# Performance work log

Hardware: AMD Instinct MI355X
Metric: run time of the kernel (lower is better)

## Reference

```python
import jax, jax.numpy as jnp
import numpy as np

N_NODES = 100000
N_EDGES = 1600000
F_IN = 128
HIDDEN = 128
N_CLASSES = 2
N_GRAPHS = 512


def setup_inputs() -> dict:
    key = jax.random.key(0)
    ks = jax.random.split(key, 10)
    node_features = jax.random.normal(ks[0], (N_NODES, F_IN), dtype=jnp.float32)
    edge_index = jax.random.randint(ks[1], (2, N_EDGES), 0, N_NODES, dtype=jnp.int64)
    batch = jnp.sort(jax.random.randint(ks[2], (N_NODES,), 0, N_GRAPHS, dtype=jnp.int64))
    s1 = 1.0 / np.sqrt(F_IN)
    s2 = 1.0 / np.sqrt(HIDDEN)
    W1 = jax.random.uniform(ks[3], (F_IN, HIDDEN), jnp.float32, -s1, s1)
    b1 = jnp.zeros((HIDDEN,), jnp.float32)
    W2 = jax.random.uniform(ks[4], (HIDDEN, HIDDEN), jnp.float32, -s2, s2)
    b2 = jnp.zeros((HIDDEN,), jnp.float32)
    Wlin = jax.random.uniform(ks[5], (HIDDEN, N_CLASSES), jnp.float32, -s2, s2)
    blin = jax.random.uniform(ks[6], (N_CLASSES,), jnp.float32, -s2, s2)
    return {"node_features": node_features, "edge_index": edge_index, "batch": batch,
            "W1": W1, "b1": b1, "W2": W2, "b2": b2, "Wlin": Wlin, "blin": blin}


def _gcn_conv(x, src, dst, norm, W, b, n_nodes):
    # transform-then-propagate (PyG GCNConv default)
    h = x @ W                                   # [N, H]
    msg = h[src] * norm[:, None]                # gather + edge scale
    out = jax.ops.segment_sum(msg, dst, num_segments=n_nodes)  # scatter-add
    return out + b


def reference(node_features, edge_index, batch, W1, b1, W2, b2, Wlin, blin):
    n = node_features.shape[0]
    loop = jnp.arange(n, dtype=edge_index.dtype)
    src = jnp.concatenate([edge_index[0], loop])  # add self-loops
    dst = jnp.concatenate([edge_index[1], loop])
    # symmetric degree normalization: deg counts incoming edges incl. self-loop
    deg = jax.ops.segment_sum(jnp.ones_like(src, dtype=node_features.dtype), dst, num_segments=n)
    dis = jnp.where(deg > 0, jax.lax.rsqrt(jnp.maximum(deg, 1.0)), 0.0)
    norm = dis[src] * dis[dst]

    x = jax.nn.relu(_gcn_conv(node_features, src, dst, norm, W1, b1, n))
    x = jax.nn.relu(_gcn_conv(x, src, dst, norm, W2, b2, n))

    # global mean pool over graphs
    ones = jnp.ones((n,), dtype=x.dtype)
    counts = jax.ops.segment_sum(ones, batch, num_segments=N_GRAPHS)
    sums = jax.ops.segment_sum(x, batch, num_segments=N_GRAPHS)
    pooled = sums / jnp.maximum(counts, 1.0)[:, None]

    # dropout is identity in eval mode
    return pooled @ Wlin + blin
```

## Files before the change

### kernel.cpp

```cpp
#include <hip/hip_runtime.h>
#include <hip/hip_bf16.h>
#include <hip/hip_fp16.h>

constexpr int NN = 100000;
constexpr int NE = 1600000;
constexpr int NG = 512;
constexpr int F  = 128;

constexpr int NB   = 392;
constexpr int RCAP = 4608;
constexpr int CAP  = 32;
constexpr int NCH  = 8;
constexpr int BINB = 512;
constexpr int GEMB = (NN + 127) / 128;

typedef _Float16 f16;
typedef f16 f16x2 __attribute__((ext_vector_type(2)));
typedef f16 f16x4 __attribute__((ext_vector_type(4)));
typedef f16 f16x8 __attribute__((ext_vector_type(8)));
typedef float f32x4 __attribute__((ext_vector_type(4)));
typedef unsigned int u32;
typedef u32 u32x4a __attribute__((ext_vector_type(4), aligned(4)));

__global__ __launch_bounds__(256) void k1_bin_prepw(const int* __restrict__ ei,
                                                    int* __restrict__ gcur,
                                                    u32* __restrict__ binned,
                                                    const float* __restrict__ W1,
                                                    const float* __restrict__ W2,
                                                    f16* __restrict__ WT1,
                                                    f16* __restrict__ WT2) {
    __shared__ u32 stage[NB][CAP];
    __shared__ int scnt[NB];
    if (blockIdx.x >= BINB) {
        int idx = (blockIdx.x - BINB) * 256 + threadIdx.x;
        int n = idx >> 7, k = idx & 127;
        WT1[idx] = (f16)W1[k * 128 + n];
        WT2[idx] = (f16)W2[k * 128 + n];
        return;
    }
    for (int b = threadIdx.x; b < NB; b += 256) scnt[b] = 0;
    __syncthreads();
    const int per = NE / BINB;
    const int e0 = blockIdx.x * per;
    for (int r = 0; r < per; r += 256) {
        int k = r + threadIdx.x;
        if (k < per) {
            int e = e0 + k;
            int s = __builtin_nontemporal_load(&ei[e]);
            int d = __builtin_nontemporal_load(&ei[NE + e]);
            int b = d >> 8;
            u32 v = ((u32)(d & 255) << 24) | (u32)s;
            int p = atomicAdd(&scnt[b], 1);
            if (p < CAP) stage[b][p] = v;
        }
        __syncthreads();
        for (int b2 = threadIdx.x; b2 < NB; b2 += 256) {
            int n = scnt[b2];
            if (n >= 16) {
                int f = n & ~15;
                int base = b2 * RCAP + atomicAdd(&gcur[b2], f);
                const u32x4a* st4 = (const u32x4a*)&stage[b2][0];
                u32x4a* out4 = (u32x4a*)&binned[base];
                for (int j = 0; j < (f >> 2); j++) out4[j] = st4[j];
                for (int j = 0; j < n - f; j++) stage[b2][j] = stage[b2][f + j];
                scnt[b2] = n - f;
            }
        }
        __syncthreads();
    }
    for (int b2 = threadIdx.x; b2 < NB; b2 += 256) {
        int n = scnt[b2];
        if (n > 0) {
            int base = b2 * RCAP + atomicAdd(&gcur[b2], n);
            for (int j = 0; j < n; j++) binned[base + j] = stage[b2][j];
        }
    }
}

template<bool IN_HALF, bool SCALE>
__device__ __forceinline__ void gemm_body(int bid, int tid,
                                          const void* __restrict__ Xv,
                                          const f16* __restrict__ WT,
                                          const float* __restrict__ dis,
                                          f16* __restrict__ H, int M) {
    const int wid = tid >> 6;
    const int lane = tid & 63;
    const int row0 = bid * 128;
    const int wrow = wid * 32;
    const int lr = lane & 15;
    const int lk = (lane >> 4) * 8;
    f32x4 acc[2][8] = {};
    #pragma unroll
    for (int ks = 0; ks < 4; ks++) {
        f16x8 a[2], b[8];
        #pragma unroll
        for (int mf = 0; mf < 2; mf++) {
            int row = row0 + wrow + mf * 16 + lr;
            row = row < M ? row : M - 1;
            if (IN_HALF) {
                a[mf] = *(const f16x8*)((const f16*)Xv + (size_t)row * 128 + ks * 32 + lk);
            } else {
                const float* Xf = (const float*)Xv + (size_t)row * 128 + ks * 32 + lk;
                float4 v0 = *(const float4*)Xf;
                float4 v1 = *(const float4*)(Xf + 4);
                a[mf] = f16x8{(f16)v0.x, (f16)v0.y, (f16)v0.z, (f16)v0.w,
                              (f16)v1.x, (f16)v1.y, (f16)v1.z, (f16)v1.w};
            }
        }
        #pragma unroll
        for (int nf = 0; nf < 8; nf++)
            b[nf] = *(const f16x8*)(WT + (size_t)(nf * 16 + lr) * 128 + ks * 32 + lk);
        #pragma unroll
        for (int mf = 0; mf < 2; mf++)
            #pragma unroll
            for (int nf = 0; nf < 8; nf++)
                acc[mf][nf] = __builtin_amdgcn_mfma_f32_16x16x32_f16(a[mf], b[nf], acc[mf][nf], 0, 0, 0);
    }
    const int crow = (lane >> 4) * 4;
    #pragma unroll
    for (int mf = 0; mf < 2; mf++) {
        #pragma unroll
        for (int reg = 0; reg < 4; reg++) {
            int row = row0 + wrow + mf * 16 + crow + reg;
            if (row < M) {
                float sc = SCALE ? dis[row] : 1.0f;
                #pragma unroll
                for (int nf = 0; nf < 8; nf++)
                    H[(size_t)row * 128 + nf * 16 + lr] = (f16)(acc[mf][nf][reg] * sc);
            }
        }
    }
}

__global__ __launch_bounds__(256) void k2_csr_gemm1(const u32* __restrict__ binned,
                                                    const int* __restrict__ gcur,
                                                    int* __restrict__ offs,
                                                    float* __restrict__ dis,
                                                    int* __restrict__ csr_src,
                                                    const float* __restrict__ X,
                                                    const f16* __restrict__ WT1,
                                                    f16* __restrict__ H) {
    __shared__ u32 ed[RCAP];
    __shared__ u32 lcsr[RCAP];
    __shared__ int hist[256];
    __shared__ int loff[256];
    __shared__ int lcur[256];
    if (blockIdx.x >= NB) {
        gemm_body<false, false>(blockIdx.x - NB, threadIdx.x, X, WT1, nullptr, H, NN);
        return;
    }
    const int b = blockIdx.x;
    const int t = threadIdx.x;
    {
        int c0 = (t < b) ? gcur[t] : 0;
        int c1 = (t + 256 < b) ? gcur[t + 256] : 0;
        loff[t] = c0 + c1;
        __syncthreads();
        for (int d = 128; d > 0; d >>= 1) {
            if (t < d) loff[t] += loff[t + d];
            __syncthreads();
        }
    }
    const int gbase = loff[0];
    __syncthreads();
    int cnt = gcur[b];
    if (cnt > RCAP) cnt = RCAP;
    hist[t] = 0;
    if (b == 0 && t == 0) offs[NN] = NE;
    __syncthreads();
    for (int j = t; j < cnt; j += 256) {
        u32 v = __builtin_nontemporal_load(&binned[(size_t)b * RCAP + j]);
        ed[j] = v;
        atomicAdd(&hist[v >> 24], 1);
    }
    __syncthreads();
    int h = hist[t];
    loff[t] = h;
    __syncthreads();
    for (int d = 1; d < 256; d <<= 1) {
        int x = (t >= d) ? loff[t - d] : 0;
        __syncthreads();
        loff[t] += x;
        __syncthreads();
    }
    int excl = loff[t] - h;
    lcur[t] = excl;
    int node = (b << 8) + t;
    if (node < NN) {
        offs[node] = gbase + excl;
        dis[node] = rsqrtf((float)(h + 1));
    }
    __syncthreads();
    for (int j = t; j < cnt; j += 256) {
        u32 v = ed[j];
        int p = atomicAdd(&lcur[v >> 24], 1);
        lcsr[p] = v & 0x1FFFFu;
    }
    __syncthreads();
    for (int j = t; j < cnt; j += 256) csr_src[gbase + j] = (int)lcsr[j];
}

__device__ __forceinline__ void gather_rows_scaled(const f16* __restrict__ h, int i,
                                                   const int* __restrict__ offs,
                                                   const int* __restrict__ csr_src,
                                                   const float* __restrict__ dis,
                                                   int q, int r, float acc[8]) {
    if (q == 0) {
        f16x8 v = *(const f16x8*)(h + (size_t)i * F + r * 8);
        float di = dis[i];
        #pragma unroll
        for (int j = 0; j < 8; j++) acc[j] = (float)v[j] * di;
    }
    const int s = offs[i], e = offs[i + 1];
    int t = s + q;
    for (; t + 4 < e; t += 8) {
        int sr0 = csr_src[t];
        int sr1 = csr_src[t + 4];
        float d0 = dis[sr0], d1 = dis[sr1];
        f16x8 v0 = *(const f16x8*)(h + (size_t)sr0 * F + r * 8);
        f16x8 v1 = *(const f16x8*)(h + (size_t)sr1 * F + r * 8);
        #pragma unroll
        for (int j = 0; j < 8; j++)
            acc[j] += (float)v0[j] * d0 + (float)v1[j] * d1;
    }
    if (t < e) {
        int sr = csr_src[t];
        float d0 = dis[sr];
        f16x8 v = *(const f16x8*)(h + (size_t)sr * F + r * 8);
        #pragma unroll
        for (int j = 0; j < 8; j++) acc[j] += (float)v[j] * d0;
    }
    #pragma unroll
    for (int j = 0; j < 8; j++) {
        acc[j] += __shfl_xor(acc[j], 16);
        acc[j] += __shfl_xor(acc[j], 32);
    }
}

__device__ __forceinline__ void gather_rows(const f16* __restrict__ h, int i,
                                            const int* __restrict__ offs,
                                            const int* __restrict__ csr_src,
                                            int q, int r, float acc[8]) {
    if (q == 0) {
        f16x8 v = *(const f16x8*)(h + (size_t)i * F + r * 8);
        #pragma unroll
        for (int j = 0; j < 8; j++) acc[j] = (float)v[j];
    }
    const int s = offs[i], e = offs[i + 1];
    int t = s + q;
    for (; t + 4 < e; t += 8) {
        int sr0 = csr_src[t];
        int sr1 = csr_src[t + 4];
        f16x8 v0 = *(const f16x8*)(h + (size_t)sr0 * F + r * 8);
        f16x8 v1 = *(const f16x8*)(h + (size_t)sr1 * F + r * 8);
        #pragma unroll
        for (int j = 0; j < 8; j++) acc[j] += (float)v0[j] + (float)v1[j];
    }
    if (t < e) {
        int sr = csr_src[t];
        f16x8 v = *(const f16x8*)(h + (size_t)sr * F + r * 8);
        #pragma unroll
        for (int j = 0; j < 8; j++) acc[j] += (float)v[j];
    }
    #pragma unroll
    for (int j = 0; j < 8; j++) {
        acc[j] += __shfl_xor(acc[j], 16);
        acc[j] += __shfl_xor(acc[j], 32);
    }
}

__global__ __launch_bounds__(256) void aggregate_l1(const f16* __restrict__ h,
                                                    const int* __restrict__ offs,
                                                    const int* __restrict__ csr_src,
                                                    const float* __restrict__ dis,
                                                    const float* __restrict__ bias,
                                                    f16* __restrict__ out, int n) {
    int i = blockIdx.x * 4 + (threadIdx.x >> 6);
    if (i >= n) return;
    const int lane = threadIdx.x & 63;
    const int q = lane >> 4;
    const int r = lane & 15;
    float acc[8] = {};
    gather_rows_scaled(h, i, offs, csr_src, dis, q, r, acc);
    if (q == 0) {
        float di = dis[i];
        const float4* b4 = (const float4*)bias;
        float4 bb0 = b4[r * 2], bb1 = b4[r * 2 + 1];
        float bb[8] = {bb0.x, bb0.y, bb0.z, bb0.w, bb1.x, bb1.y, bb1.z, bb1.w};
        f16x8 o;
        #pragma unroll
        for (int j = 0; j < 8; j++) {
            float v = fmaf(acc[j], di, bb[j]);
            o[j] = (f16)(v > 0.f ? v : 0.f);
        }
        *(f16x8*)(out + (size_t)i * F + r * 8) = o;
    }
}

__global__ __launch_bounds__(256) void aggregate_l2(const f16* __restrict__ h,
                                                    const int* __restrict__ offs,
                                                    const int* __restrict__ csr_src,
                                                    const float* __restrict__ dis,
                                                    const float* __restrict__ bias,
                                                    f16* __restrict__ out, int n) {
    int i = blockIdx.x * 4 + (threadIdx.x >> 6);
    if (i >= n) return;
    const int lane = threadIdx.x & 63;
    const int q = lane >> 4;
    const int r = lane & 15;
    float acc[8] = {};
    gather_rows(h, i, offs, csr_src, q, r, acc);
    if (q == 0) {
        float di = dis[i];
        const float4* b4 = (const float4*)bias;
        float4 bb0 = b4[r * 2], bb1 = b4[r * 2 + 1];
        float bb[8] = {bb0.x, bb0.y, bb0.z, bb0.w, bb1.x, bb1.y, bb1.z, bb1.w};
        f16x8 o;
        #pragma unroll
        for (int j = 0; j < 8; j++) {
            float v = fmaf(acc[j], di, bb[j]);
            o[j] = (f16)(v > 0.f ? v : 0.f);
        }
        *(f16x8*)(out + (size_t)i * F + r * 8) = o;
    }
}

__global__ __launch_bounds__(256) void gemm2(const f16* __restrict__ Xh,
                                             const f16* __restrict__ WT,
                                             const float* __restrict__ dis,
                                             f16* __restrict__ H, int M) {
    gemm_body<true, true>(blockIdx.x, threadIdx.x, Xh, WT, dis, H, M);
}

__global__ __launch_bounds__(256) void pool_partial(const f16* __restrict__ x,
                                                    const int* __restrict__ batch,
                                                    float* __restrict__ partial, int n) {
    int g = blockIdx.x;
    __shared__ int se[2];
    if (threadIdx.x < 2) {
        int target = g + threadIdx.x;
        int lo = 0, hi = n;
        while (lo < hi) {
            int mid = (lo + hi) >> 1;
            if (batch[mid] < target) lo = mid + 1; else hi = mid;
        }
        se[threadIdx.x] = lo;
    }
    __syncthreads();
    int s = se[0], e = se[1];
    int wid = threadIdx.x >> 6, lane = threadIdx.x & 63;
    int slot = blockIdx.y * 4 + wid;
    float a0 = 0.f, a1 = 0.f;
    const f16x2* x2 = (const f16x2*)x;
    for (int i = s + slot; i < e; i += 4 * NCH) {
        f16x2 v = x2[(size_t)i * 64 + lane];
        a0 += (float)v[0];
        a1 += (float)v[1];
    }
    __shared__ float red[4][128];
    red[wid][lane * 2] = a0;
    red[wid][lane * 2 + 1] = a1;
    __syncthreads();
    if (wid == 0) {
        float s0 = red[0][lane * 2] + red[1][lane * 2] + red[2][lane * 2] + red[3][lane * 2];
        float s1 = red[0][lane * 2 + 1] + red[1][lane * 2 + 1] + red[2][lane * 2 + 1] + red[3][lane * 2 + 1];
        float2* pp = (float2*)&partial[((size_t)g * NCH + blockIdx.y) * F];
        pp[lane] = make_float2(s0, s1);
    }
}

__global__ __launch_bounds__(128) void pool_final(const float* __restrict__ partial,
                                                  const int* __restrict__ batch,
                                                  const float* __restrict__ Wlin,
                                                  const float* __restrict__ blin,
                                                  float* __restrict__ out, int n) {
    int g = blockIdx.x;
    int f = threadIdx.x;
    __shared__ int se[2];
    if (threadIdx.x < 2) {
        int target = g + threadIdx.x;
        int lo = 0, hi = n;
        while (lo < hi) {
            int mid = (lo + hi) >> 1;
            if (batch[mid] < target) lo = mid + 1; else hi = mid;
        }
        se[threadIdx.x] = lo;
    }
    __syncthreads();
    int s = se[0], e = se[1];
    float acc = 0.f;
    #pragma unroll
    for (int c = 0; c < NCH; c++) acc += partial[((size_t)g * NCH + c) * F + f];
    float cnt = (float)((e - s) > 0 ? (e - s) : 1);
    float p = acc / cnt;
    float v0 = p * Wlin[f * 2 + 0];
    float v1 = p * Wlin[f * 2 + 1];
    #pragma unroll
    for (int o = 32; o > 0; o >>= 1) {
        v0 += __shfl_xor(v0, o);
        v1 += __shfl_xor(v1, o);
    }
    __shared__ float red[4];
    int wid = threadIdx.x >> 6;
    if ((threadIdx.x & 63) == 0) { red[wid * 2] = v0; red[wid * 2 + 1] = v1; }
    __syncthreads();
    if (threadIdx.x == 0) {
        out[g * 2 + 0] = red[0] + red[2] + blin[0];
        out[g * 2 + 1] = red[1] + red[3] + blin[1];
    }
}

extern "C" void kernel_launch(void* const* d_in, const int* in_sizes, int n_in,
                              void* d_out, int out_size, void* d_ws, size_t ws_size,
                              hipStream_t stream) {
    const float* X     = (const float*)d_in[0];
    const int*   ei    = (const int*)d_in[1];
    const int*   batch = (const int*)d_in[2];
    const float* W1    = (const float*)d_in[3];
    const float* b1    = (const float*)d_in[4];
    const float* W2    = (const float*)d_in[5];
    const float* b2    = (const float*)d_in[6];
    const float* Wlin  = (const float*)d_in[7];
    const float* blin  = (const float*)d_in[8];
    float* out = (float*)d_out;

    char* p = (char*)d_ws;
    auto alloc = [&](size_t bytes) -> char* {
        char* r = p;
        p += (bytes + 255) & ~size_t(255);
        return r;
    };
    int*   gcur       = (int*)alloc((size_t)NB * 4);
    int*   offs       = (int*)alloc((size_t)(NN + 1) * 4);
    float* dis        = (float*)alloc((size_t)NN * 4);
    u32*   binned     = (u32*)alloc((size_t)NB * RCAP * 4);
    int*   csr_src    = (int*)alloc((size_t)NE * 4);
    f16*   WT1        = (f16*)alloc((size_t)128 * 128 * 2);
    f16*   WT2        = (f16*)alloc((size_t)128 * 128 * 2);
    f16*   bufA       = (f16*)alloc((size_t)NN * F * 2);
    f16*   bufB       = (f16*)alloc((size_t)NN * F * 2);
    float* partial    = (float*)alloc((size_t)NG * NCH * F * 4);

    hipMemsetAsync(gcur, 0, (size_t)NB * 4, stream);
    k1_bin_prepw<<<BINB + 64, 256, 0, stream>>>(ei, gcur, binned, W1, W2, WT1, WT2);
    k2_csr_gemm1<<<NB + GEMB, 256, 0, stream>>>(binned, gcur, offs, dis, csr_src,
                                                X, WT1, bufA);
    aggregate_l1<<<(NN + 3) / 4, 256, 0, stream>>>(bufA, offs, csr_src, dis, b1, bufB, NN);
    gemm2<<<GEMB, 256, 0, stream>>>(bufB, WT2, dis, bufA, NN);
    aggregate_l2<<<(NN + 3) / 4, 256, 0, stream>>>(bufA, offs, csr_src, dis, b2, bufB, NN);
    pool_partial<<<dim3(NG, NCH), 256, 0, stream>>>(bufB, batch, partial, NN);
    pool_final<<<NG, 128, 0, stream>>>(partial, batch, Wlin, blin, out, NN);
}
```

Before: 252.3 us.

## Move layer-1 GEMM into binning kernel with per-block LDS weight transpose

The layer-1 feature GEMM moves out of the CSR-build kernel and into the first (edge-binning) kernel. Each GEMM block now transposes W1 into padded shared memory itself instead of reading a pre-transposed global WT1, which removes the dependency on a prior transpose. The binning and GEMM work run concurrently, and the CSR kernel becomes a small launch of its own. In exchange, every GEMM block redoes the W1 transpose, and the kernel's shared-memory footprint (about 51 KB) may limit occupancy for all its block types.

After: 252.6 us. About the same (+0.1%).

```diff
diff --git a/kernel.cpp b/kernel.cpp
--- a/kernel.cpp
+++ b/kernel.cpp
@@ -13,6 +13,7 @@
 constexpr int NCH  = 8;
 constexpr int BINB = 512;
 constexpr int GEMB = (NN + 127) / 128;
+constexpr int PWB  = 32;
 
 typedef _Float16 f16;
 typedef f16 f16x2 __attribute__((ext_vector_type(2)));
@@ -22,28 +23,99 @@
 typedef unsigned int u32;
 typedef u32 u32x4a __attribute__((ext_vector_type(4), aligned(4)));
 
-__global__ __launch_bounds__(256) void k1_bin_prepw(const int* __restrict__ ei,
-                                                    int* __restrict__ gcur,
-                                                    u32* __restrict__ binned,
-                                                    const float* __restrict__ W1,
-                                                    const float* __restrict__ W2,
-                                                    f16* __restrict__ WT1,
-                                                    f16* __restrict__ WT2) {
-    __shared__ u32 stage[NB][CAP];
-    __shared__ int scnt[NB];
+__global__ __launch_bounds__(256) void k1_fused(const int* __restrict__ ei,
+                                                int* __restrict__ gcur,
+                                                u32* __restrict__ binned,
+                                                const float* __restrict__ W1,
+                                                const float* __restrict__ W2,
+                                                f16* __restrict__ WT2,
+                                                const float* __restrict__ X,
+                                                f16* __restrict__ H) {
+    __shared__ char smem[51744];
+    const int tid = threadIdx.x;
+
+    if (blockIdx.x >= BINB + GEMB) {
+        int base = (blockIdx.x - BINB - GEMB) * 512;
+        #pragma unroll
+        for (int u = 0; u < 2; u++) {
+            int idx = base + u * 256 + tid;
+            int n = idx >> 7, k = idx & 127;
+            WT2[idx] = (f16)W2[k * 128 + n];
+        }
+        return;
+    }
+
     if (blockIdx.x >= BINB) {
-        int idx = (blockIdx.x - BINB) * 256 + threadIdx.x;
-        int n = idx >> 7, k = idx & 127;
-        WT1[idx] = (f16)W1[k * 128 + n];
-        WT2[idx] = (f16)W2[k * 128 + n];
+        f16* sW = (f16*)smem;
+        {
+            const float4* W4 = (const float4*)W1;
+            #pragma unroll
+            for (int i = 0; i < 16; i++) {
+                int idx = tid + 256 * i;
+                int k = idx >> 5;
+                int n0 = (idx & 31) * 4;
+                float4 v = W4[idx];
+                sW[(n0 + 0) * 136 + k] = (f16)v.x;
+                sW[(n0 + 1) * 136 + k] = (f16)v.y;
+                sW[(n0 + 2) * 136 + k] = (f16)v.z;
+                sW[(n0 + 3) * 136 + k] = (f16)v.w;
+            }
+        }
+        __syncthreads();
+        const int bid = blockIdx.x - BINB;
+        const int wid = tid >> 6;
+        const int lane = tid & 63;
+        const int row0 = bid * 128;
+        const int wrow = wid * 32;
+        const int lr = lane & 15;
+        const int lk = (lane >> 4) * 8;
+        f32x4 acc[2][8] = {};
+        #pragma unroll
+        for (int ks = 0; ks < 4; ks++) {
+            f16x8 a[2], b[8];
+            #pragma unroll
+            for (int mf = 0; mf < 2; mf++) {
+                int row = row0 + wrow + mf * 16 + lr;
+                row = row < NN ? row : NN - 1;
+                const float* Xf = X + (size_t)row * 128 + ks * 32 + lk;
+                float4 v0 = *(const float4*)Xf;
+                float4 v1 = *(const float4*)(Xf + 4);
+                a[mf] = f16x8{(f16)v0.x, (f16)v0.y, (f16)v0.z, (f16)v0.w,
+                              (f16)v1.x, (f16)v1.y, (f16)v1.z, (f16)v1.w};
+            }
+            #pragma unroll
+            for (int nf = 0; nf < 8; nf++)
+                b[nf] = *(const f16x8*)&sW[(nf * 16 + lr) * 136 + ks * 32 + lk];
+            #pragma unroll
+            for (int mf = 0; mf < 2; mf++)
+                #pragma unroll
+                for (int nf = 0; nf < 8; nf++)
+                    acc[mf][nf] = __builtin_amdgcn_mfma_f32_16x16x32_f16(a[mf], b[nf], acc[mf][nf], 0, 0, 0);
+        }
+        const int crow = (lane >> 4) * 4;
+        #pragma unroll
+        for (int mf = 0; mf < 2; mf++) {
+            #pragma unroll
+            for (int reg = 0; reg < 4; reg++) {
+                int row = row0 + wrow + mf * 16 + crow + reg;
+                if (row < NN) {
+                    #pragma unroll
+                    for (int nf = 0; nf < 8; nf++)
+                        H[(size_t)row * 128 + nf * 16 + lr] = (f16)acc[mf][nf][reg];
+                }
+            }
+        }
         return;
     }
-    for (int b = threadIdx.x; b < NB; b += 256) scnt[b] = 0;
+
+    u32 (*stage)[CAP] = (u32(*)[CAP])smem;
+    int* scnt = (int*)(smem + NB * CAP * 4);
+    for (int b = tid; b < NB; b += 256) scnt[b] = 0;
     __syncthreads();
     const int per = NE / BINB;
     const int e0 = blockIdx.x * per;
     for (int r = 0; r < per; r += 256) {
-        int k = r + threadIdx.x;
+        int k = r + tid;
         if (k < per) {
             int e = e0 + k;
             int s = __builtin_nontemporal_load(&ei[e]);
@@ -54,7 +126,7 @@
             if (p < CAP) stage[b][p] = v;
         }
         __syncthreads();
-        for (int b2 = threadIdx.x; b2 < NB; b2 += 256) {
+        for (int b2 = tid; b2 < NB; b2 += 256) {
             int n = scnt[b2];
             if (n >= 16) {
                 int f = n & ~15;
@@ -68,7 +140,7 @@
         }
         __syncthreads();
     }
-    for (int b2 = threadIdx.x; b2 < NB; b2 += 256) {
+    for (int b2 = tid; b2 < NB; b2 += 256) {
         int n = scnt[b2];
         if (n > 0) {
             int base = b2 * RCAP + atomicAdd(&gcur[b2], n);
@@ -77,78 +149,16 @@
     }
 }
 
-template<bool IN_HALF, bool SCALE>
-__device__ __forceinline__ void gemm_body(int bid, int tid,
-                                          const void* __restrict__ Xv,
-                                          const f16* __restrict__ WT,
-                                          const float* __restrict__ dis,
-                                          f16* __restrict__ H, int M) {
-    const int wid = tid >> 6;
-    const int lane = tid & 63;
-    const int row0 = bid * 128;
-    const int wrow = wid * 32;
-    const int lr = lane & 15;
-    const int lk = (lane >> 4) * 8;
-    f32x4 acc[2][8] = {};
-    #pragma unroll
-    for (int ks = 0; ks < 4; ks++) {
-        f16x8 a[2], b[8];
-        #pragma unroll
-        for (int mf = 0; mf < 2; mf++) {
-            int row = row0 + wrow + mf * 16 + lr;
-            row = row < M ? row : M - 1;
-            if (IN_HALF) {
-                a[mf] = *(const f16x8*)((const f16*)Xv + (size_t)row * 128 + ks * 32 + lk);
-            } else {
-                const float* Xf = (const float*)Xv + (size_t)row * 128 + ks * 32 + lk;
-                float4 v0 = *(const float4*)Xf;
-                float4 v1 = *(const float4*)(Xf + 4);
-                a[mf] = f16x8{(f16)v0.x, (f16)v0.y, (f16)v0.z, (f16)v0.w,
-                              (f16)v1.x, (f16)v1.y, (f16)v1.z, (f16)v1.w};
-            }
-        }
-        #pragma unroll
-        for (int nf = 0; nf < 8; nf++)
-            b[nf] = *(const f16x8*)(WT + (size_t)(nf * 16 + lr) * 128 + ks * 32 + lk);
-        #pragma unroll
-        for (int mf = 0; mf < 2; mf++)
-            #pragma unroll
-            for (int nf = 0; nf < 8; nf++)
-                acc[mf][nf] = __builtin_amdgcn_mfma_f32_16x16x32_f16(a[mf], b[nf], acc[mf][nf], 0, 0, 0);
-    }
-    const int crow = (lane >> 4) * 4;
-    #pragma unroll
-    for (int mf = 0; mf < 2; mf++) {
-        #pragma unroll
-        for (int reg = 0; reg < 4; reg++) {
-            int row = row0 + wrow + mf * 16 + crow + reg;
-            if (row < M) {
-                float sc = SCALE ? dis[row] : 1.0f;
-                #pragma unroll
-                for (int nf = 0; nf < 8; nf++)
-                    H[(size_t)row * 128 + nf * 16 + lr] = (f16)(acc[mf][nf][reg] * sc);
-            }
-        }
-    }
-}
-
-__global__ __launch_bounds__(256) void k2_csr_gemm1(const u32* __restrict__ binned,
-                                                    const int* __restrict__ gcur,
-                                                    int* __restrict__ offs,
-                                                    float* __restrict__ dis,
-                                                    int* __restrict__ csr_src,
-                                                    const float* __restrict__ X,
-                                                    const f16* __restrict__ WT1,
-                                                    f16* __restrict__ H) {
+__global__ __launch_bounds__(256) void k2_csr(const u32* __restrict__ binned,
+                                              const int* __restrict__ gcur,
+                                              int* __restrict__ offs,
+                                              float* __restrict__ dis,
+                                              int* __restrict__ csr_src) {
     __shared__ u32 ed[RCAP];
     __shared__ u32 lcsr[RCAP];
     __shared__ int hist[256];
     __shared__ int loff[256];
     __shared__ int lcur[256];
-    if (blockIdx.x >= NB) {
-        gemm_body<false, false>(blockIdx.x - NB, threadIdx.x, X, WT1, nullptr, H, NN);
-        return;
-    }
     const int b = blockIdx.x;
     const int t = threadIdx.x;
     {
@@ -198,6 +208,52 @@
     }
     __syncthreads();
     for (int j = t; j < cnt; j += 256) csr_src[gbase + j] = (int)lcsr[j];
+}
+
+__global__ __launch_bounds__(256) void gemm2(const f16* __restrict__ Xh,
+                                             const f16* __restrict__ WT,
+                                             const float* __restrict__ dis,
+                                             f16* __restrict__ H, int M) {
+    const int tid = threadIdx.x;
+    const int wid = tid >> 6;
+    const int lane = tid & 63;
+    const int row0 = blockIdx.x * 128;
+    const int wrow = wid * 32;
+    const int lr = lane & 15;
+    const int lk = (lane >> 4) * 8;
+    f32x4 acc[2][8] = {};
+    #pragma unroll
+    for (int ks = 0; ks < 4; ks++) {
+        f16x8 a[2], b[8];
+        #pragma unroll
+        for (int mf = 0; mf < 2; mf++) {
+            int row = row0 + wrow + mf * 16 + lr;
+            row = row < M ? row : M - 1;
+            a[mf] = *(const f16x8*)(Xh + (size_t)row * 128 + ks * 32 + lk);
+        }
+        #pragma unroll
+        for (int nf = 0; nf < 8; nf++)
+            b[nf] = *(const f16x8*)(WT + (size_t)(nf * 16 + lr) * 128 + ks * 32 + lk);
+        #pragma unroll
+        for (int mf = 0; mf < 2; mf++)
+            #pragma unroll
+            for (int nf = 0; nf < 8; nf++)
+                acc[mf][nf] = __builtin_amdgcn_mfma_f32_16x16x32_f16(a[mf], b[nf], acc[mf][nf], 0, 0, 0);
+    }
+    const int crow = (lane >> 4) * 4;
+    #pragma unroll
+    for (int mf = 0; mf < 2; mf++) {
+        #pragma unroll
+        for (int reg = 0; reg < 4; reg++) {
+            int row = row0 + wrow + mf * 16 + crow + reg;
+            if (row < M) {
+                float sc = dis[row];
+                #pragma unroll
+                for (int nf = 0; nf < 8; nf++)
+                    H[(size_t)row * 128 + nf * 16 + lr] = (f16)(acc[mf][nf][reg] * sc);
+            }
+        }
+    }
 }
 
 __device__ __forceinline__ void gather_rows_scaled(const f16* __restrict__ h, int i,
@@ -325,13 +381,6 @@
     }
 }
 
-__global__ __launch_bounds__(256) void gemm2(const f16* __restrict__ Xh,
-                                             const f16* __restrict__ WT,
-                                             const float* __restrict__ dis,
-                                             f16* __restrict__ H, int M) {
-    gemm_body<true, true>(blockIdx.x, threadIdx.x, Xh, WT, dis, H, M);
-}
-
 __global__ __launch_bounds__(256) void pool_partial(const f16* __restrict__ x,
                                                     const int* __restrict__ batch,
                                                     float* __restrict__ partial, int n) {
@@ -435,16 +484,14 @@
     float* dis        = (float*)alloc((size_t)NN * 4);
     u32*   binned     = (u32*)alloc((size_t)NB * RCAP * 4);
     int*   csr_src    = (int*)alloc((size_t)NE * 4);
-    f16*   WT1        = (f16*)alloc((size_t)128 * 128 * 2);
     f16*   WT2        = (f16*)alloc((size_t)128 * 128 * 2);
     f16*   bufA       = (f16*)alloc((size_t)NN * F * 2);
     f16*   bufB       = (f16*)alloc((size_t)NN * F * 2);
     float* partial    = (float*)alloc((size_t)NG * NCH * F * 4);
 
     hipMemsetAsync(gcur, 0, (size_t)NB * 4, stream);
-    k1_bin_prepw<<<BINB + 64, 256, 0, stream>>>(ei, gcur, binned, W1, W2, WT1, WT2);
-    k2_csr_gemm1<<<NB + GEMB, 256, 0, stream>>>(binned, gcur, offs, dis, csr_src,
-                                                X, WT1, bufA);
+    k1_fused<<<BINB + GEMB + PWB, 256, 0, stream>>>(ei, gcur, binned, W1, W2, WT2, X, bufA);
+    k2_csr<<<NB, 256, 0, stream>>>(binned, gcur, offs, dis, csr_src);
     aggregate_l1<<<(NN + 3) / 4, 256, 0, stream>>>(bufA, offs, csr_src, dis, b1, bufB, NN);
     gemm2<<<GEMB, 256, 0, stream>>>(bufB, WT2, dis, bufA, NN);
     aggregate_l2<<<(NN + 3) / 4, 256, 0, stream>>>(bufA, offs, csr_src, dis, b2, bufB, NN);
```
